# Performance work log

Hardware: AMD Instinct MI355X
Metric: run time of the kernel (lower is better)

Reference implementation:

```python
import jax, jax.numpy as jnp
import numpy as np

B, S, H, P, L, O, E = 32, 1024, 256, 96, 200, 200, 64
N_EULER = 4


def setup_inputs() -> dict:
    key = jax.random.key(0)
    ks = jax.random.split(key, 20)
    def w(k, shape, fan_in):
        return jax.random.normal(k, shape, dtype=jnp.float32) / np.float32(np.sqrt(fan_in))
    return {
        'eco_data': jax.random.normal(ks[0], (B, E), dtype=jnp.float32),
        'tran_data': jax.random.normal(ks[1], (B, S, H), dtype=jnp.float32),
        'tran_data_label': jax.random.normal(ks[2], (B, P, 1), dtype=jnp.float32),
        'time_x': jax.random.uniform(ks[3], (B, S, 1), dtype=jnp.float32),
        'time_y': jax.random.uniform(ks[4], (B, P, 1), dtype=jnp.float32),
        'alpha': jnp.ones((1,), dtype=jnp.float32),
        'W_eco': w(ks[5], (E, H), E), 'b_eco': jnp.zeros((H,), jnp.float32),
        'W_in': w(ks[6], (3, H, L), H), 'W_t': w(ks[7], (3, 1, L), 1), 'b_in': jnp.zeros((3, L), jnp.float32),
        'W_f1': w(ks[8], (3, L, O), L), 'b_f1': jnp.zeros((3, O), jnp.float32),
        'W_f2': w(ks[9], (3, O, L), O), 'b_f2': jnp.zeros((3, L), jnp.float32),
        'W_out': w(ks[10], (3, L, H), L), 'b_out': jnp.zeros((3, H), jnp.float32),
        'W_lin': w(ks[11], (H, P), H), 'b_lin': jnp.zeros((P,), jnp.float32),
    }


def reference(eco_data, tran_data, tran_data_label, time_x, time_y, alpha,
              W_eco, b_eco, W_in, W_t, b_in, W_f1, b_f1, W_f2, b_f2,
              W_out, b_out, W_lin, b_lin):
    S_ = tran_data.shape[1]
    # eco_model: linear encoder [B, E] -> [B, H]
    eco_vec = eco_data @ W_eco + b_eco
    # time features over the observed window (concat then slice, per original)
    time_f = jnp.concatenate([time_x, time_y], axis=1)[:, :S_, :]  # [B, S, 1]
    # ODE_RNN for Q/K/V, stacked on k=3: encode -> Euler ODE solve -> readout
    h = jnp.tanh(jnp.einsum('bsh,khl->kbsl', tran_data, W_in)
                 + jnp.einsum('bst,ktl->kbsl', time_f, W_t)
                 + b_in[:, None, None, :])  # [3, B, S, L]
    dt = jnp.float32(1.0 / N_EULER)
    for _ in range(N_EULER):  # fixed-step Euler solve of tanh-MLP vector field
        hid = jnp.tanh(jnp.einsum('kbsl,klo->kbso', h, W_f1) + b_f1[:, None, None, :])
        f = jnp.einsum('kbso,kol->kbsl', hid, W_f2) + b_f2[:, None, None, :]
        h = h + dt * f
    qkv = (jnp.einsum('kbsl,klh->kbsh', h, W_out) + b_out[:, None, None, :]
           + eco_vec[None, :, None, :])  # [3, B, S, H]
    # zero out padded timesteps (last channel == 0 means padding)
    mask = jnp.where(tran_data[:, :, -1] == 0, 0.0, 1.0)[None, :, :, None]
    qkv = qkv * mask
    Q, K, V = qkv[0], qkv[1], qkv[2]
    scale = jnp.float32(1.0 / np.sqrt(H))
    scores = jnp.einsum('bqh,bkh->bqk', Q, K) * scale  # [B, S, S]
    attn = jax.nn.softmax(scores, axis=-1)
    ctx = jnp.einsum('bqk,bkh->bqh', attn, V)  # [B, S, H]
    out = ctx @ W_lin + b_lin  # [B, S, P]
    return out
```

## Files before the change

kernel.cpp:

```cpp
#include <hip/hip_runtime.h>

constexpr int Bc = 32, Sc = 1024, Hc = 256, Pc = 96, Lc = 200, Oc = 200, Ec = 64;
constexpr int Mtot = Bc * Sc;
constexpr float DT = 0.25f;
constexpr int KP = 224;

enum { MODE_ENC = 0, MODE_QKV = 3, MODE_OUT = 4, MODE_BF16OUT = 5 };

typedef short bf16x8 __attribute__((ext_vector_type(8)));
typedef float f32x4 __attribute__((ext_vector_type(4)));
typedef unsigned short u16x8 __attribute__((ext_vector_type(8)));

__device__ inline unsigned short f2bf(float x) {
    union { float f; unsigned int u; } v; v.f = x;
    unsigned int r = v.u + 0x7FFFu + ((v.u >> 16) & 1u);
    return (unsigned short)(r >> 16);
}
__device__ inline float bf2f(unsigned short x) {
    union { unsigned int u; float f; } v; v.u = ((unsigned int)x) << 16;
    return v.f;
}
__device__ inline float fast_tanh(float x) {
    float cx = fminf(fmaxf(x, -15.f), 15.f);
    float e = __expf(2.f * cx);
    return __fdividef(e - 1.f, e + 1.f);
}

__global__ __launch_bounds__(256) void eco_kernel(
    const float* __restrict__ eco_data, const float* __restrict__ W_eco,
    const float* __restrict__ b_eco, float* __restrict__ eco_vec)
{
    const int b = blockIdx.x, h = threadIdx.x;
    float acc = b_eco[h];
    #pragma unroll
    for (int e = 0; e < Ec; e++)
        acc = fmaf(eco_data[b * Ec + e], W_eco[(size_t)e * Hc + h], acc);
    eco_vec[(size_t)b * Hc + h] = acc;
}

__global__ void wtrans_all(
    const float* __restrict__ W_in, const float* __restrict__ W_f1,
    const float* __restrict__ W_f2, const float* __restrict__ W_out,
    const float* __restrict__ W_lin,
    unsigned short* __restrict__ WinT, unsigned short* __restrict__ Wf1T,
    unsigned short* __restrict__ Wf2T, unsigned short* __restrict__ WoutT,
    unsigned short* __restrict__ WlinT)
{
    const int z = blockIdx.z;
    const int n = blockIdx.x * 16 + threadIdx.x;
    const int k = blockIdx.y * 16 + threadIdx.y;

    const float* W; unsigned short* WT;
    int K, N, Kpad, Npad;
    if (z < 3)       { W = W_in  + (size_t)z * 256 * 200;       WT = WinT  + (size_t)z * 256 * 256;       K = 256; N = 200; Kpad = 256; Npad = 256; }
    else if (z < 6)  { W = W_f1  + (size_t)(z - 3) * 200 * 200; WT = Wf1T  + (size_t)(z - 3) * 224 * 256; K = 200; N = 200; Kpad = 224; Npad = 256; }
    else if (z < 9)  { W = W_f2  + (size_t)(z - 6) * 200 * 200; WT = Wf2T  + (size_t)(z - 6) * 224 * 256; K = 200; N = 200; Kpad = 224; Npad = 256; }
    else if (z < 12) { W = W_out + (size_t)(z - 9) * 200 * 256; WT = WoutT + (size_t)(z - 9) * 224 * 256; K = 200; N = 256; Kpad = 224; Npad = 256; }
    else             { W = W_lin;                               WT = WlinT;                               K = 256; N =  96; Kpad = 256; Npad = 128; }

    if (n >= Npad || k >= Kpad) return;
    float v = (n < N && k < K) ? W[(size_t)k * N + n] : 0.f;
    WT[(size_t)n * Kpad + k] = f2bf(v);
}

template <int MODE, typename TA>
__global__ __launch_bounds__(256) void mfma_gemm(
    const TA* __restrict__ A, const unsigned short* __restrict__ WT,
    const float* __restrict__ bias, void* __restrict__ Cv,
    int M, int N, int K, int Kpad,
    size_t aStrideZ, size_t wStrideZ, size_t bStrideZ, size_t cStrideZ,
    const float* __restrict__ timev, const float* __restrict__ wtv,
    const float* __restrict__ eco, const float* __restrict__ trandat,
    unsigned short* __restrict__ Ck, unsigned short* __restrict__ Cvt)
{
    constexpr int LDS_S = 40;
    __shared__ unsigned short SM[128 * LDS_S * 2];
    unsigned short* As = SM;
    unsigned short* Bs = SM + 128 * LDS_S;

    const int tid = threadIdx.x;
    const int z = blockIdx.z;
    const int m0 = blockIdx.y * 128;
    const int n0 = blockIdx.x * 128;

    A    += (size_t)z * aStrideZ;
    WT   += (size_t)z * wStrideZ;
    bias += (size_t)z * bStrideZ;
    float* Cf = (float*)Cv + (size_t)z * cStrideZ;
    unsigned short* Cu = (unsigned short*)Cv + (size_t)z * cStrideZ;
    const float* wtp = wtv ? (wtv + (size_t)z * Lc) : nullptr;

    const int lane = tid & 63, wave = tid >> 6;
    const int wm = (wave & 1) * 64, wn = (wave >> 1) * 64;
    const int fm = lane & 15, fq = lane >> 4;

    f32x4 acc[4][4];
    #pragma unroll
    for (int i = 0; i < 4; i++)
        #pragma unroll
        for (int j = 0; j < 4; j++)
            acc[i][j] = (f32x4){0.f, 0.f, 0.f, 0.f};

    for (int k0 = 0; k0 < K; k0 += 32) {
        if (k0) __syncthreads();
        #pragma unroll
        for (int i = 0; i < 4; i++) {
            const int f = i * 256 + tid;
            const int row = f >> 3, kq = f & 7;
            const int k = k0 + kq * 4;
            ushort4 s;
            if constexpr (sizeof(TA) == 4) {
                float4 v = {0.f, 0.f, 0.f, 0.f};
                if (k < K) v = *(const float4*)((const float*)A + (size_t)(m0 + row) * K + k);
                s.x = f2bf(v.x); s.y = f2bf(v.y); s.z = f2bf(v.z); s.w = f2bf(v.w);
            } else {
                s = make_ushort4(0, 0, 0, 0);
                if (k < K) s = *(const ushort4*)((const unsigned short*)A + (size_t)(m0 + row) * K + k);
            }
            *(ushort4*)&As[row * LDS_S + kq * 4] = s;
        }
        #pragma unroll
        for (int i = 0; i < 2; i++) {
            const int f = i * 256 + tid;
            const int row = f >> 2, q = f & 3;
            u16x8 v = *(const u16x8*)(WT + (size_t)(n0 + row) * Kpad + k0 + q * 8);
            *(u16x8*)&Bs[row * LDS_S + q * 8] = v;
        }
        __syncthreads();

        bf16x8 af[4], bfr[4];
        #pragma unroll
        for (int mi = 0; mi < 4; mi++)
            af[mi] = *(const bf16x8*)&As[(wm + mi * 16 + fm) * LDS_S + fq * 8];
        #pragma unroll
        for (int nj = 0; nj < 4; nj++)
            bfr[nj] = *(const bf16x8*)&Bs[(wn + nj * 16 + fm) * LDS_S + fq * 8];
        #pragma unroll
        for (int mi = 0; mi < 4; mi++)
            #pragma unroll
            for (int nj = 0; nj < 4; nj++)
                acc[mi][nj] = __builtin_amdgcn_mfma_f32_16x16x32_bf16(
                    af[mi], bfr[nj], acc[mi][nj], 0, 0, 0);
    }

    if (MODE == MODE_QKV && z == 2) {
        constexpr int BSTR = 136;
        const int bq = m0 >> 10, sq0 = m0 & (Sc - 1);
        const int myhalf = wn >> 6;
        #pragma unroll
        for (int half = 0; half < 2; half++) {
            __syncthreads();
            if (myhalf == half) {
                #pragma unroll
                for (int mi = 0; mi < 4; mi++)
                    #pragma unroll
                    for (int nj = 0; nj < 4; nj++) {
                        const int nn = n0 + wn + nj * 16 + fm;
                        const float bv = bias[nn];
                        const float ev = eco[(size_t)bq * Hc + nn];
                        #pragma unroll
                        for (int r = 0; r < 4; r++) {
                            const int mm = m0 + wm + mi * 16 + fq * 4 + r;
                            float v = acc[mi][nj][r] + bv + ev;
                            if (trandat[(size_t)mm * Hc + (Hc - 1)] == 0.f) v = 0.f;
                            SM[(nj * 16 + fm) * BSTR + wm + mi * 16 + fq * 4 + r] = f2bf(v);
                        }
                    }
            }
            __syncthreads();
            #pragma unroll
            for (int i = 0; i < 4; i++) {
                const int vv = i * 256 + tid;
                const int nl = vv >> 4, vc = vv & 15;
                *(u16x8*)&Cvt[((size_t)bq * Hc + n0 + half * 64 + nl) * Sc + sq0 + vc * 8] =
                    *(const u16x8*)&SM[nl * BSTR + vc * 8];
            }
        }
        return;
    }

    #pragma unroll
    for (int mi = 0; mi < 4; mi++) {
        #pragma unroll
        for (int nj = 0; nj < 4; nj++) {
            const int nn = n0 + wn + nj * 16 + fm;
            if (nn >= N) continue;
            const float bv = (MODE == MODE_BF16OUT) ? 0.f
                           : ((MODE == MODE_ENC && nn >= Lc) ? 0.f : bias[nn]);
            #pragma unroll
            for (int r = 0; r < 4; r++) {
                const int mm = m0 + wm + mi * 16 + fq * 4 + r;
                float v = acc[mi][nj][r] + bv;
                if (MODE == MODE_ENC) {
                    float vv = (nn < Lc) ? fast_tanh(v + timev[mm] * wtp[nn]) : 0.f;
                    Cu[(size_t)mm * N + nn] = f2bf(vv);
                } else if (MODE == MODE_QKV) {
                    v += eco[(size_t)(mm >> 10) * Hc + nn];
                    if (trandat[(size_t)mm * Hc + (Hc - 1)] == 0.f) v = 0.f;
                    if (z == 0)      ((unsigned short*)Cv)[(size_t)mm * Hc + nn] = f2bf(v * 0.0625f);
                    else             Ck[(size_t)mm * Hc + nn] = f2bf(v);
                } else if (MODE == MODE_BF16OUT) {
                    Cu[(size_t)mm * N + nn] = f2bf(v);
                } else {
                    Cf[(size_t)mm * N + nn] = v;
                }
            }
        }
    }
}

__global__ __launch_bounds__(512, 2) void euler_fused(
    unsigned short* __restrict__ hg,
    const unsigned short* __restrict__ W1,
    const unsigned short* __restrict__ W2,
    const float* __restrict__ b1g, const float* __restrict__ b2g)
{
    constexpr int HS = 232;
    constexpr int WS = 40;
    extern __shared__ unsigned short lds[];
    unsigned short* hs  = lds;
    unsigned short* wsb[2] = { lds + 29696, lds + 38656 };
    unsigned short* hcb[2] = { lds + 47616, lds + 52736 };

    const int tid = threadIdx.x;
    const int z = blockIdx.y;
    const int m0 = blockIdx.x * 128;
    unsigned short* hrow = hg + ((size_t)z * Mtot + m0) * KP;
    const unsigned short* W1z = W1 + (size_t)z * 256 * KP;
    const unsigned short* W2z = W2 + (size_t)z * 256 * KP;

    const int lane = tid & 63, w = tid >> 6;
    const int wm = (w & 3) * 32, wn = (w >> 2) * 112;
    const int fm = lane & 15, fq = lane >> 4;

    const int sr = tid >> 2, sq = tid & 3;
    const bool s2 = (tid < 384);

    float b1r[7], b2r[7];
    #pragma unroll
    for (int nj = 0; nj < 7; nj++) {
        const int nn = wn + nj * 16 + fm;
        b1r[nj] = (nn < Oc) ? b1g[z * Oc + nn] : 0.f;
        b2r[nj] = (nn < Lc) ? b2g[z * Lc + nn] : 0.f;
    }

    u16x8 pr0, pr1;
    pr0 = *(const u16x8*)&W1z[sr * KP + sq * 8];
    if (s2) pr1 = *(const u16x8*)&W1z[(sr + 128) * KP + sq * 8];

    #pragma unroll
    for (int i = 0; i < 7; i++) {
        const int f = i * 512 + tid;
        const int r = f / 28, c = (f % 28) * 8;
        *(u16x8*)&hs[r * HS + c] = *(const u16x8*)&hrow[(size_t)r * KP + c];
    }

    for (int it = 0; it < 4; it++) {
        __syncthreads();
        *(u16x8*)&wsb[0][sr * WS + sq * 8] = pr0;
        if (s2) *(u16x8*)&wsb[0][(sr + 128) * WS + sq * 8] = pr1;
        pr0 = *(const u16x8*)&W1z[sr * KP + 32 + sq * 8];
        if (s2) pr1 = *(const u16x8*)&W1z[(sr + 128) * KP + 32 + sq * 8];
        __syncthreads();

        f32x4 acc[2][7];
        #pragma unroll
        for (int mi = 0; mi < 2; mi++)
            #pragma unroll
            for (int nj = 0; nj < 7; nj++)
                acc[mi][nj] = (f32x4){0.f, 0.f, 0.f, 0.f};

        for (int k = 0; k < 7; k++) {
            if (k < 6) {
                unsigned short* wb = wsb[(k + 1) & 1];
                *(u16x8*)&wb[sr * WS + sq * 8] = pr0;
                if (s2) *(u16x8*)&wb[(sr + 128) * WS + sq * 8] = pr1;
                const unsigned short* src = (k + 2 < 7) ? (W1z + (k + 2) * 32) : W2z;
                pr0 = *(const u16x8*)&src[sr * KP + sq * 8];
                if (s2) pr1 = *(const u16x8*)&src[(sr + 128) * KP + sq * 8];
            }
            const unsigned short* wr = wsb[k & 1];
            bf16x8 af[2], bfr[7];
            #pragma unroll
            for (int mi = 0; mi < 2; mi++)
                af[mi] = *(const bf16x8*)&hs[(wm + mi * 16 + fm) * HS + k * 32 + fq * 8];
            #pragma unroll
            for (int nj = 0; nj < 7; nj++)
                bfr[nj] = *(const bf16x8*)&wr[(wn + nj * 16 + fm) * WS + fq * 8];
            #pragma unroll
            for (int mi = 0; mi < 2; mi++)
                #pragma unroll
                for (int nj = 0; nj < 7; nj++)
                    acc[mi][nj] = __builtin_amdgcn_mfma_f32_16x16x32_bf16(
                        af[mi], bfr[nj], acc[mi][nj], 0, 0, 0);
            __syncthreads();
        }

        unsigned short hidp[2][7][4];
        #pragma unroll
        for (int mi = 0; mi < 2; mi++)
            #pragma unroll
            for (int nj = 0; nj < 7; nj++)
                #pragma unroll
                for (int r = 0; r < 4; r++)
                    hidp[mi][nj][r] = f2bf(fast_tanh(acc[mi][nj][r] + b1r[nj]));

        {
            *(u16x8*)&wsb[0][sr * WS + sq * 8] = pr0;
            if (s2) *(u16x8*)&wsb[0][(sr + 128) * WS + sq * 8] = pr1;
            pr0 = *(const u16x8*)&W2z[sr * KP + 32 + sq * 8];
            if (s2) pr1 = *(const u16x8*)&W2z[(sr + 128) * KP + 32 + sq * 8];
            #pragma unroll
            for (int t2 = 0; t2 < 2; t2++) {
                const int c0 = t2 * 16;
                if (c0 >= wn && c0 < wn + 112) {
                    const int nj = (c0 - wn) >> 4;
                    #pragma unroll
                    for (int mi = 0; mi < 2; mi++)
                        #pragma unroll
                        for (int r = 0; r < 4; r++)
                            hcb[0][(wm + mi * 16 + fq * 4 + r) * WS + t2 * 16 + fm] =
                                hidp[mi][nj][r];
                }
            }
        }
        __syncthreads();

        f32x4 fac[2][7];
        #pragma unroll
        for (int mi = 0; mi < 2; mi++)
            #pragma unroll
            for (int nj = 0; nj < 7; nj++)
                fac[mi][nj] = (f32x4){0.f, 0.f, 0.f, 0.f};

        for (int k = 0; k < 7; k++) {
            if (k < 6) {
                unsigned short* wb = wsb[(k + 1) & 1];
                unsigned short* hb = hcb[(k + 1) & 1];
                *(u16x8*)&wb[sr * WS + sq * 8] = pr0;
                if (s2) *(u16x8*)&wb[(sr + 128) * WS + sq * 8] = pr1;
                if (k + 2 < 7) {
                    pr0 = *(const u16x8*)&W2z[sr * KP + (k + 2) * 32 + sq * 8];
                    if (s2) pr1 = *(const u16x8*)&W2z[(sr + 128) * KP + (k + 2) * 32 + sq * 8];
                } else if (it != 3) {
                    pr0 = *(const u16x8*)&W1z[sr * KP + sq * 8];
                    if (s2) pr1 = *(const u16x8*)&W1z[(sr + 128) * KP + sq * 8];
                }
                #pragma unroll
                for (int t2 = 0; t2 < 2; t2++) {
                    const int c0 = (k + 1) * 32 + t2 * 16;
                    if (c0 >= wn && c0 < wn + 112) {
                        const int nj = (c0 - wn) >> 4;
                        #pragma unroll
                        for (int mi = 0; mi < 2; mi++)
                            #pragma unroll
                            for (int r = 0; r < 4; r++)
                                hb[(wm + mi * 16 + fq * 4 + r) * WS + t2 * 16 + fm] =
                                    hidp[mi][nj][r];
                    }
                }
            }
            const unsigned short* wr = wsb[k & 1];
            const unsigned short* hr = hcb[k & 1];
            bf16x8 af2[2], bf2[7];
            #pragma unroll
            for (int mi = 0; mi < 2; mi++)
                af2[mi] = *(const bf16x8*)&hr[(wm + mi * 16 + fm) * WS + fq * 8];
            #pragma unroll
            for (int nj = 0; nj < 7; nj++)
                bf2[nj] = *(const bf16x8*)&wr[(wn + nj * 16 + fm) * WS + fq * 8];
            #pragma unroll
            for (int mi = 0; mi < 2; mi++)
                #pragma unroll
                for (int nj = 0; nj < 7; nj++)
                    fac[mi][nj] = __builtin_amdgcn_mfma_f32_16x16x32_bf16(
                        af2[mi], bf2[nj], fac[mi][nj], 0, 0, 0);
            __syncthreads();
        }

        #pragma unroll
        for (int mi = 0; mi < 2; mi++)
            #pragma unroll
            for (int nj = 0; nj < 7; nj++) {
                const int nn = wn + nj * 16 + fm;
                #pragma unroll
                for (int r = 0; r < 4; r++) {
                    const int row = wm + mi * 16 + fq * 4 + r;
                    const float fv = fac[mi][nj][r] + b2r[nj];
                    hs[row * HS + nn] = f2bf(bf2f(hs[row * HS + nn]) + DT * fv);
                }
            }
    }

    __syncthreads();
    #pragma unroll
    for (int i = 0; i < 7; i++) {
        const int f = i * 512 + tid;
        const int r = f / 28, c = (f % 28) * 8;
        *(u16x8*)&hrow[(size_t)r * KP + c] = *(const u16x8*)&hs[r * HS + c];
    }
}

__global__ __launch_bounds__(512) void flash_attn(
    const unsigned short* __restrict__ Qb, const unsigned short* __restrict__ Kb,
    const unsigned short* __restrict__ VT, unsigned short* __restrict__ ctx)
{
    constexpr int QS = 264;
    constexpr int KS = 264;
    constexpr int VS = 72;
    constexpr int PS = 72;
    extern __shared__ unsigned short lds[];
    unsigned short* qs = lds;
    unsigned short* ks = lds + 128 * QS;
    unsigned short* vs = lds + 128 * QS + 64 * KS;
    unsigned short* ps = lds + 128 * QS + 64 * KS + 256 * VS;

    const int tid = threadIdx.x;
    const int b = blockIdx.y, q0 = blockIdx.x * 128;
    const int lane = tid & 63, w = tid >> 6;
    const int fm = lane & 15, fq = lane >> 4;
    unsigned short* psw = ps + w * 16 * PS;

    const unsigned short* Qp = Qb + (size_t)b * Sc * Hc;
    const unsigned short* Kp = Kb + (size_t)b * Sc * Hc;
    const unsigned short* Vp = VT + (size_t)b * Hc * Sc;

    #pragma unroll
    for (int i = 0; i < 8; i++) {
        const int v = i * 512 + tid;
        *(u16x8*)&qs[(v >> 5) * QS + (v & 31) * 8] =
            *(const u16x8*)&Qp[(size_t)(q0 + (v >> 5)) * Hc + (v & 31) * 8];
    }

    f32x4 of[16];
    #pragma unroll
    for (int nj = 0; nj < 16; nj++) of[nj] = (f32x4){0.f, 0.f, 0.f, 0.f};
    float lrun[4] = {0.f, 0.f, 0.f, 0.f};

    for (int c = 0; c < 16; c++) {
        __syncthreads();
        const int s0 = c * 64;
        #pragma unroll
        for (int i = 0; i < 4; i++) {
            const int v = i * 512 + tid;
            *(u16x8*)&ks[(v >> 5) * KS + (v & 31) * 8] =
                *(const u16x8*)&Kp[(size_t)(s0 + (v >> 5)) * Hc + (v & 31) * 8];
            *(u16x8*)&vs[(v >> 3) * VS + (v & 7) * 8] =
                *(const u16x8*)&Vp[(size_t)(v >> 3) * Sc + s0 + (v & 7) * 8];
        }
        __syncthreads();

        f32x4 sc[4];
        #pragma unroll
        for (int nj = 0; nj < 4; nj++) sc[nj] = (f32x4){0.f, 0.f, 0.f, 0.f};
        #pragma unroll
        for (int kc = 0; kc < 8; kc++) {
            const bf16x8 aq = *(const bf16x8*)&qs[(w * 16 + fm) * QS + kc * 32 + fq * 8];
            #pragma unroll
            for (int nj = 0; nj < 4; nj++) {
                const bf16x8 bk = *(const bf16x8*)&ks[(nj * 16 + fm) * KS + kc * 32 + fq * 8];
                sc[nj] = __builtin_amdgcn_mfma_f32_16x16x32_bf16(aq, bk, sc[nj], 0, 0, 0);
            }
        }

        float rsum[4] = {0.f, 0.f, 0.f, 0.f};
        #pragma unroll
        for (int nj = 0; nj < 4; nj++)
            #pragma unroll
            for (int r = 0; r < 4; r++) {
                const float p = __expf(sc[nj][r]);
                rsum[r] += p;
                psw[(fq * 4 + r) * PS + nj * 16 + fm] = f2bf(p);
            }
        #pragma unroll
        for (int r = 0; r < 4; r++) {
            float s = rsum[r];
            #pragma unroll
            for (int o = 8; o > 0; o >>= 1) s += __shfl_xor(s, o, 64);
            lrun[r] += s;
        }

        #pragma unroll
        for (int t = 0; t < 2; t++) {
            const bf16x8 ap = *(const bf16x8*)&psw[fm * PS + t * 32 + fq * 8];
            #pragma unroll
            for (int nj = 0; nj < 16; nj++) {
                const bf16x8 bv = *(const bf16x8*)&vs[(nj * 16 + fm) * VS + t * 32 + fq * 8];
                of[nj] = __builtin_amdgcn_mfma_f32_16x16x32_bf16(ap, bv, of[nj], 0, 0, 0);
            }
        }
    }

    float inv[4];
    #pragma unroll
    for (int r = 0; r < 4; r++) inv[r] = __frcp_rn(lrun[r]);
    #pragma unroll
    for (int nj = 0; nj < 16; nj++)
        #pragma unroll
        for (int r = 0; r < 4; r++)
            ctx[((size_t)b * Sc + q0 + w * 16 + fq * 4 + r) * Hc + nj * 16 + fm] =
                f2bf(of[nj][r] * inv[r]);
}

extern "C" void kernel_launch(void* const* d_in, const int* in_sizes, int n_in,
                              void* d_out, int out_size, void* d_ws, size_t ws_size,
                              hipStream_t stream)
{
    const float* eco_data = (const float*)d_in[0];
    const float* tran     = (const float*)d_in[1];
    const float* time_x   = (const float*)d_in[3];
    const float* W_eco    = (const float*)d_in[6];
    const float* b_eco    = (const float*)d_in[7];
    const float* W_in     = (const float*)d_in[8];
    const float* W_t      = (const float*)d_in[9];
    const float* b_in     = (const float*)d_in[10];
    const float* W_f1     = (const float*)d_in[11];
    const float* b_f1     = (const float*)d_in[12];
    const float* W_f2     = (const float*)d_in[13];
    const float* b_f2     = (const float*)d_in[14];
    const float* W_out    = (const float*)d_in[15];
    const float* b_out    = (const float*)d_in[16];
    const float* W_lin    = (const float*)d_in[17];
    const float* b_lin    = (const float*)d_in[18];
    float* out = (float*)d_out;

    float* eco_vec = (float*)d_ws;
    unsigned short* hpad = (unsigned short*)(eco_vec + 8192);
    unsigned short* Qb = hpad + (size_t)3 * Mtot * KP;
    unsigned short* Kb = Qb + (size_t)Mtot * Hc;
    unsigned short* VT = Kb + (size_t)Mtot * Hc;
    unsigned short* P  = VT + (size_t)Mtot * Hc;
    unsigned short* WinT  = P + (size_t)Mtot * Sc;
    unsigned short* Wf1T  = WinT  + (size_t)3 * 256 * 256;
    unsigned short* Wf2T  = Wf1T  + (size_t)3 * 256 * KP;
    unsigned short* WoutT = Wf2T  + (size_t)3 * 256 * KP;
    unsigned short* WlinT = WoutT + (size_t)3 * 256 * KP;
    unsigned short* ctxb = hpad;

    constexpr int EULER_LDS = 57856 * 2;
    static_assert(EULER_LDS == 115712, "euler lds");
    hipFuncSetAttribute((const void*)euler_fused,
                        hipFuncAttributeMaxDynamicSharedMemorySize, EULER_LDS);
    constexpr int FLASH_LDS = (128 * 264 + 64 * 264 + 256 * 72 + 8 * 16 * 72) * 2;
    static_assert(FLASH_LDS == 156672, "flash lds");
    hipFuncSetAttribute((const void*)flash_attn,
                        hipFuncAttributeMaxDynamicSharedMemorySize, FLASH_LDS);

    eco_kernel<<<Bc, Hc, 0, stream>>>(eco_data, W_eco, b_eco, eco_vec);

    wtrans_all<<<dim3(16, 16, 13), dim3(16, 16), 0, stream>>>(
        W_in, W_f1, W_f2, W_out, W_lin, WinT, Wf1T, Wf2T, WoutT, WlinT);

    const dim3 blk(256);

    mfma_gemm<MODE_ENC, float><<<dim3(2, 256, 3), blk, 0, stream>>>(
        tran, WinT, b_in, hpad, Mtot, KP, Hc, 256,
        0, 65536, Lc, (size_t)Mtot * KP, time_x, W_t, nullptr, nullptr, nullptr, nullptr);

    euler_fused<<<dim3(Mtot / 128, 3), 512, EULER_LDS, stream>>>(
        hpad, Wf1T, Wf2T, b_f1, b_f2);

    mfma_gemm<MODE_QKV, unsigned short><<<dim3(2, 256, 3), blk, 0, stream>>>(
        hpad, WoutT, b_out, Qb, Mtot, Hc, KP, KP,
        (size_t)Mtot * KP, 57344, Hc, 0, nullptr, nullptr, eco_vec, tran, Kb, VT);

    flash_attn<<<dim3(8, 32), 512, FLASH_LDS, stream>>>(Qb, Kb, VT, ctxb);

    mfma_gemm<MODE_OUT, unsigned short><<<dim3(1, 256, 1), blk, 0, stream>>>(
        ctxb, WlinT, b_lin, out, Mtot, Pc, Hc, 256,
        0, 0, 0, 0, nullptr, nullptr, nullptr, nullptr, nullptr, nullptr);
}
```

Measured before the change: 521.5 us.

## Halve Euler kernel row tile to 64 and move biases to LDS for occupancy

The fused Euler kernel now processes 64 rows per block instead of 128, so each wave handles one 16-row MFMA tile instead of two. Accumulator and bias registers drop, and the biases move into shared memory, shrinking LDS from about 113KB to 76KB. Launch bounds are raised to allow more blocks per CU. The cost is that every weight tile streamed through LDS is now reused across half as many rows, which doubles weight traffic and barrier count per row.

```diff
diff --git a/kernel.cpp b/kernel.cpp
--- a/kernel.cpp
+++ b/kernel.cpp
@@ -209,7 +209,7 @@
     }
 }
 
-__global__ __launch_bounds__(512, 2) void euler_fused(
+__global__ __launch_bounds__(512, 4) void euler_fused(
     unsigned short* __restrict__ hg,
     const unsigned short* __restrict__ W1,
     const unsigned short* __restrict__ W2,
@@ -219,29 +219,29 @@
     constexpr int WS = 40;
     extern __shared__ unsigned short lds[];
     unsigned short* hs  = lds;
-    unsigned short* wsb[2] = { lds + 29696, lds + 38656 };
-    unsigned short* hcb[2] = { lds + 47616, lds + 52736 };
+    unsigned short* wsb[2] = { lds + 14848, lds + 23808 };
+    unsigned short* hcb[2] = { lds + 32768, lds + 35328 };
+    float* bs = (float*)(lds + 37888);
 
     const int tid = threadIdx.x;
     const int z = blockIdx.y;
-    const int m0 = blockIdx.x * 128;
+    const int m0 = blockIdx.x * 64;
     unsigned short* hrow = hg + ((size_t)z * Mtot + m0) * KP;
     const unsigned short* W1z = W1 + (size_t)z * 256 * KP;
     const unsigned short* W2z = W2 + (size_t)z * 256 * KP;
 
     const int lane = tid & 63, w = tid >> 6;
-    const int wm = (w & 3) * 32, wn = (w >> 2) * 112;
+    const int wm = (w & 3) * 16, wn = (w >> 2) * 112;
     const int fm = lane & 15, fq = lane >> 4;
 
     const int sr = tid >> 2, sq = tid & 3;
     const bool s2 = (tid < 384);
 
-    float b1r[7], b2r[7];
-    #pragma unroll
-    for (int nj = 0; nj < 7; nj++) {
-        const int nn = wn + nj * 16 + fm;
-        b1r[nj] = (nn < Oc) ? b1g[z * Oc + nn] : 0.f;
-        b2r[nj] = (nn < Lc) ? b2g[z * Lc + nn] : 0.f;
+    if (tid < 448) {
+        float v;
+        if (tid < 224) v = (tid < Oc) ? b1g[z * Oc + tid] : 0.f;
+        else { const int t = tid - 224; v = (t < Lc) ? b2g[z * Lc + t] : 0.f; }
+        bs[tid] = v;
     }
 
     u16x8 pr0, pr1;
@@ -249,10 +249,12 @@
     if (s2) pr1 = *(const u16x8*)&W1z[(sr + 128) * KP + sq * 8];
 
     #pragma unroll
-    for (int i = 0; i < 7; i++) {
+    for (int i = 0; i < 4; i++) {
         const int f = i * 512 + tid;
-        const int r = f / 28, c = (f % 28) * 8;
-        *(u16x8*)&hs[r * HS + c] = *(const u16x8*)&hrow[(size_t)r * KP + c];
+        if (f < 1792) {
+            const int r = f / 28, c = (f % 28) * 8;
+            *(u16x8*)&hs[r * HS + c] = *(const u16x8*)&hrow[(size_t)r * KP + c];
+        }
     }
 
     for (int it = 0; it < 4; it++) {
@@ -263,12 +265,10 @@
         if (s2) pr1 = *(const u16x8*)&W1z[(sr + 128) * KP + 32 + sq * 8];
         __syncthreads();
 
-        f32x4 acc[2][7];
-        #pragma unroll
-        for (int mi = 0; mi < 2; mi++)
-            #pragma unroll
-            for (int nj = 0; nj < 7; nj++)
-                acc[mi][nj] = (f32x4){0.f, 0.f, 0.f, 0.f};
+        f32x4 acc[7];
+        #pragma unroll
+        for (int nj = 0; nj < 7; nj++)
+            acc[nj] = (f32x4){0.f, 0.f, 0.f, 0.f};
 
         for (int k = 0; k < 7; k++) {
             if (k < 6) {
@@ -280,30 +280,26 @@
                 if (s2) pr1 = *(const u16x8*)&src[(sr + 128) * KP + sq * 8];
             }
             const unsigned short* wr = wsb[k & 1];
-            bf16x8 af[2], bfr[7];
-            #pragma unroll
-            for (int mi = 0; mi < 2; mi++)
-                af[mi] = *(const bf16x8*)&hs[(wm + mi * 16 + fm) * HS + k * 32 + fq * 8];
+            const bf16x8 af = *(const bf16x8*)&hs[(wm + fm) * HS + k * 32 + fq * 8];
+            bf16x8 bfr[7];
             #pragma unroll
             for (int nj = 0; nj < 7; nj++)
                 bfr[nj] = *(const bf16x8*)&wr[(wn + nj * 16 + fm) * WS + fq * 8];
             #pragma unroll
-            for (int mi = 0; mi < 2; mi++)
-                #pragma unroll
-                for (int nj = 0; nj < 7; nj++)
-                    acc[mi][nj] = __builtin_amdgcn_mfma_f32_16x16x32_bf16(
-                        af[mi], bfr[nj], acc[mi][nj], 0, 0, 0);
+            for (int nj = 0; nj < 7; nj++)
+                acc[nj] = __builtin_amdgcn_mfma_f32_16x16x32_bf16(
+                    af, bfr[nj], acc[nj], 0, 0, 0);
             __syncthreads();
         }
 
-        unsigned short hidp[2][7][4];
-        #pragma unroll
-        for (int mi = 0; mi < 2; mi++)
-            #pragma unroll
-            for (int nj = 0; nj < 7; nj++)
-                #pragma unroll
-                for (int r = 0; r < 4; r++)
-                    hidp[mi][nj][r] = f2bf(fast_tanh(acc[mi][nj][r] + b1r[nj]));
+        unsigned short hidp[7][4];
+        #pragma unroll
+        for (int nj = 0; nj < 7; nj++) {
+            const float b1v = bs[wn + nj * 16 + fm];
+            #pragma unroll
+            for (int r = 0; r < 4; r++)
+                hidp[nj][r] = f2bf(fast_tanh(acc[nj][r] + b1v));
+        }
 
         {
             *(u16x8*)&wsb[0][sr * WS + sq * 8] = pr0;
@@ -316,22 +312,17 @@
                 if (c0 >= wn && c0 < wn + 112) {
                     const int nj = (c0 - wn) >> 4;
                     #pragma unroll
-                    for (int mi = 0; mi < 2; mi++)
-                        #pragma unroll
-                        for (int r = 0; r < 4; r++)
-                            hcb[0][(wm + mi * 16 + fq * 4 + r) * WS + t2 * 16 + fm] =
-                                hidp[mi][nj][r];
+                    for (int r = 0; r < 4; r++)
+                        hcb[0][(wm + fq * 4 + r) * WS + t2 * 16 + fm] = hidp[nj][r];
                 }
             }
         }
         __syncthreads();
 
-        f32x4 fac[2][7];
-        #pragma unroll
-        for (int mi = 0; mi < 2; mi++)
-            #pragma unroll
-            for (int nj = 0; nj < 7; nj++)
-                fac[mi][nj] = (f32x4){0.f, 0.f, 0.f, 0.f};
+        f32x4 fac[7];
+        #pragma unroll
+        for (int nj = 0; nj < 7; nj++)
+            fac[nj] = (f32x4){0.f, 0.f, 0.f, 0.f};
 
         for (int k = 0; k < 7; k++) {
             if (k < 6) {
@@ -352,52 +343,46 @@
                     if (c0 >= wn && c0 < wn + 112) {
                         const int nj = (c0 - wn) >> 4;
                         #pragma unroll
-                        for (int mi = 0; mi < 2; mi++)
-                            #pragma unroll
-                            for (int r = 0; r < 4; r++)
-                                hb[(wm + mi * 16 + fq * 4 + r) * WS + t2 * 16 + fm] =
-                                    hidp[mi][nj][r];
+                        for (int r = 0; r < 4; r++)
+                            hb[(wm + fq * 4 + r) * WS + t2 * 16 + fm] = hidp[nj][r];
                     }
                 }
             }
             const unsigned short* wr = wsb[k & 1];
             const unsigned short* hr = hcb[k & 1];
-            bf16x8 af2[2], bf2[7];
-            #pragma unroll
-            for (int mi = 0; mi < 2; mi++)
-                af2[mi] = *(const bf16x8*)&hr[(wm + mi * 16 + fm) * WS + fq * 8];
+            const bf16x8 af2 = *(const bf16x8*)&hr[(wm + fm) * WS + fq * 8];
+            bf16x8 bf2[7];
             #pragma unroll
             for (int nj = 0; nj < 7; nj++)
                 bf2[nj] = *(const bf16x8*)&wr[(wn + nj * 16 + fm) * WS + fq * 8];
             #pragma unroll
-            for (int mi = 0; mi < 2; mi++)
-                #pragma unroll
-                for (int nj = 0; nj < 7; nj++)
-                    fac[mi][nj] = __builtin_amdgcn_mfma_f32_16x16x32_bf16(
-                        af2[mi], bf2[nj], fac[mi][nj], 0, 0, 0);
+            for (int nj = 0; nj < 7; nj++)
+                fac[nj] = __builtin_amdgcn_mfma_f32_16x16x32_bf16(
+                    af2, bf2[nj], fac[nj], 0, 0, 0);
             __syncthreads();
         }
 
         #pragma unroll
-        for (int mi = 0; mi < 2; mi++)
-            #pragma unroll
-            for (int nj = 0; nj < 7; nj++) {
-                const int nn = wn + nj * 16 + fm;
-                #pragma unroll
-                for (int r = 0; r < 4; r++) {
-                    const int row = wm + mi * 16 + fq * 4 + r;
-                    const float fv = fac[mi][nj][r] + b2r[nj];
-                    hs[row * HS + nn] = f2bf(bf2f(hs[row * HS + nn]) + DT * fv);
-                }
-            }
+        for (int nj = 0; nj < 7; nj++) {
+            const int nn = wn + nj * 16 + fm;
+            const float b2v = bs[224 + nn];
+            #pragma unroll
+            for (int r = 0; r < 4; r++) {
+                const int row = wm + fq * 4 + r;
+                const float fv = fac[nj][r] + b2v;
+                hs[row * HS + nn] = f2bf(bf2f(hs[row * HS + nn]) + DT * fv);
+            }
+        }
     }
 
     __syncthreads();
     #pragma unroll
-    for (int i = 0; i < 7; i++) {
+    for (int i = 0; i < 4; i++) {
         const int f = i * 512 + tid;
-        const int r = f / 28, c = (f % 28) * 8;
-        *(u16x8*)&hrow[(size_t)r * KP + c] = *(const u16x8*)&hs[r * HS + c];
+        if (f < 1792) {
+            const int r = f / 28, c = (f % 28) * 8;
+            *(u16x8*)&hrow[(size_t)r * KP + c] = *(const u16x8*)&hs[r * HS + c];
+        }
     }
 }
 
@@ -537,8 +522,8 @@
     unsigned short* WlinT = WoutT + (size_t)3 * 256 * KP;
     unsigned short* ctxb = hpad;
 
-    constexpr int EULER_LDS = 57856 * 2;
-    static_assert(EULER_LDS == 115712, "euler lds");
+    constexpr int EULER_LDS = (14848 + 2 * 8960 + 2 * 2560) * 2 + 448 * 4;
+    static_assert(EULER_LDS == 77568, "euler lds");
     hipFuncSetAttribute((const void*)euler_fused,
                         hipFuncAttributeMaxDynamicSharedMemorySize, EULER_LDS);
     constexpr int FLASH_LDS = (128 * 264 + 64 * 264 + 256 * 72 + 8 * 16 * 72) * 2;
@@ -557,7 +542,7 @@
         tran, WinT, b_in, hpad, Mtot, KP, Hc, 256,
         0, 65536, Lc, (size_t)Mtot * KP, time_x, W_t, nullptr, nullptr, nullptr, nullptr);
 
-    euler_fused<<<dim3(Mtot / 128, 3), 512, EULER_LDS, stream>>>(
+    euler_fused<<<dim3(Mtot / 64, 3), 512, EULER_LDS, stream>>>(
         hpad, Wf1T, Wf2T, b_f1, b_f2);
 
     mfma_gemm<MODE_QKV, unsigned short><<<dim3(2, 256, 3), blk, 0, stream>>>(
```

Measured after the change: 568.2 us. 1.09x slower.

## Double-buffer K/V tiles in flash attention with register-resident Q

Applied to the files above, without the earlier changes.

Restructures the flash attention kernel so Q fragments stay in registers rather than LDS. K and V are streamed in 32-key chunks through a double-buffered LDS ring, with global loads for the next chunk issued before the current chunk's MFMAs. This cuts LDS footprint and leaves one barrier per iteration instead of two, aiming to hide global load latency. The trade-off is twice as many loop iterations with smaller MFMA batches and more register pressure from the prefetch and Q registers.

```diff
diff --git a/kernel.cpp b/kernel.cpp
--- a/kernel.cpp
+++ b/kernel.cpp
@@ -405,15 +405,13 @@
     const unsigned short* __restrict__ Qb, const unsigned short* __restrict__ Kb,
     const unsigned short* __restrict__ VT, unsigned short* __restrict__ ctx)
 {
-    constexpr int QS = 264;
-    constexpr int KS = 264;
-    constexpr int VS = 72;
-    constexpr int PS = 72;
+    constexpr int KS = 260;
+    constexpr int VS = 68;
+    constexpr int PS = 36;
     extern __shared__ unsigned short lds[];
-    unsigned short* qs = lds;
-    unsigned short* ks = lds + 128 * QS;
-    unsigned short* vs = lds + 128 * QS + 64 * KS;
-    unsigned short* ps = lds + 128 * QS + 64 * KS + 256 * VS;
+    unsigned short* ks = lds;
+    unsigned short* vs = lds + 2 * 32 * KS;
+    unsigned short* ps = lds + 2 * 32 * KS + 2 * 256 * VS;
 
     const int tid = threadIdx.x;
     const int b = blockIdx.y, q0 = blockIdx.x * 128;
@@ -425,53 +423,69 @@
     const unsigned short* Kp = Kb + (size_t)b * Sc * Hc;
     const unsigned short* Vp = VT + (size_t)b * Hc * Sc;
 
-    #pragma unroll
-    for (int i = 0; i < 8; i++) {
-        const int v = i * 512 + tid;
-        *(u16x8*)&qs[(v >> 5) * QS + (v & 31) * 8] =
-            *(const u16x8*)&Qp[(size_t)(q0 + (v >> 5)) * Hc + (v & 31) * 8];
-    }
+    bf16x8 aq[8];
+    #pragma unroll
+    for (int kc = 0; kc < 8; kc++)
+        aq[kc] = *(const bf16x8*)&Qp[(size_t)(q0 + w * 16 + fm) * Hc + kc * 32 + fq * 8];
+
+    const int kr = tid >> 5, kcol = (tid & 31) * 8;
+    const int vr = tid >> 2, vcol = (tid & 3) * 8;
+    const unsigned short* KgA = Kp + (size_t)kr * Hc + kcol;
+    const unsigned short* KgB = KgA + (size_t)16 * Hc;
+    const unsigned short* VgA = Vp + (size_t)vr * Sc + vcol;
+    const unsigned short* VgB = VgA + (size_t)128 * Sc;
+    const int kwA = kr * KS + kcol, kwB = (kr + 16) * KS + kcol;
+    const int vwA = vr * VS + vcol, vwB = (vr + 128) * VS + vcol;
+
+    {
+        u16x8 a0 = *(const u16x8*)KgA;
+        u16x8 a1 = *(const u16x8*)KgB;
+        u16x8 b0 = *(const u16x8*)VgA;
+        u16x8 b1 = *(const u16x8*)VgB;
+        *(u16x8*)&ks[kwA] = a0; *(u16x8*)&ks[kwB] = a1;
+        *(u16x8*)&vs[vwA] = b0; *(u16x8*)&vs[vwB] = b1;
+    }
+    __syncthreads();
 
     f32x4 of[16];
     #pragma unroll
     for (int nj = 0; nj < 16; nj++) of[nj] = (f32x4){0.f, 0.f, 0.f, 0.f};
     float lrun[4] = {0.f, 0.f, 0.f, 0.f};
 
-    for (int c = 0; c < 16; c++) {
-        __syncthreads();
-        const int s0 = c * 64;
-        #pragma unroll
-        for (int i = 0; i < 4; i++) {
-            const int v = i * 512 + tid;
-            *(u16x8*)&ks[(v >> 5) * KS + (v & 31) * 8] =
-                *(const u16x8*)&Kp[(size_t)(s0 + (v >> 5)) * Hc + (v & 31) * 8];
-            *(u16x8*)&vs[(v >> 3) * VS + (v & 7) * 8] =
-                *(const u16x8*)&Vp[(size_t)(v >> 3) * Sc + s0 + (v & 7) * 8];
-        }
-        __syncthreads();
-
-        f32x4 sc[4];
-        #pragma unroll
-        for (int nj = 0; nj < 4; nj++) sc[nj] = (f32x4){0.f, 0.f, 0.f, 0.f};
+    int cur = 0;
+    for (int c = 0; c < 32; c++) {
+        u16x8 nk0, nk1, nv0, nv1;
+        if (c < 31) {
+            const size_t ko = (size_t)(c + 1) * 32 * Hc;
+            const size_t vo = (size_t)(c + 1) * 32;
+            nk0 = *(const u16x8*)(KgA + ko);
+            nk1 = *(const u16x8*)(KgB + ko);
+            nv0 = *(const u16x8*)(VgA + vo);
+            nv1 = *(const u16x8*)(VgB + vo);
+        }
+
+        const unsigned short* ksc = ks + cur * (32 * KS);
+        const unsigned short* vsc = vs + cur * (256 * VS);
+
+        f32x4 s0v = (f32x4){0.f, 0.f, 0.f, 0.f};
+        f32x4 s1v = (f32x4){0.f, 0.f, 0.f, 0.f};
         #pragma unroll
         for (int kc = 0; kc < 8; kc++) {
-            const bf16x8 aq = *(const bf16x8*)&qs[(w * 16 + fm) * QS + kc * 32 + fq * 8];
-            #pragma unroll
-            for (int nj = 0; nj < 4; nj++) {
-                const bf16x8 bk = *(const bf16x8*)&ks[(nj * 16 + fm) * KS + kc * 32 + fq * 8];
-                sc[nj] = __builtin_amdgcn_mfma_f32_16x16x32_bf16(aq, bk, sc[nj], 0, 0, 0);
-            }
-        }
-
-        float rsum[4] = {0.f, 0.f, 0.f, 0.f};
-        #pragma unroll
-        for (int nj = 0; nj < 4; nj++)
-            #pragma unroll
-            for (int r = 0; r < 4; r++) {
-                const float p = __expf(sc[nj][r]);
-                rsum[r] += p;
-                psw[(fq * 4 + r) * PS + nj * 16 + fm] = f2bf(p);
-            }
+            const bf16x8 bk0 = *(const bf16x8*)&ksc[fm * KS + kc * 32 + fq * 8];
+            const bf16x8 bk1 = *(const bf16x8*)&ksc[(16 + fm) * KS + kc * 32 + fq * 8];
+            s0v = __builtin_amdgcn_mfma_f32_16x16x32_bf16(aq[kc], bk0, s0v, 0, 0, 0);
+            s1v = __builtin_amdgcn_mfma_f32_16x16x32_bf16(aq[kc], bk1, s1v, 0, 0, 0);
+        }
+
+        float rsum[4];
+        #pragma unroll
+        for (int r = 0; r < 4; r++) {
+            const float p0 = __expf(s0v[r]);
+            const float p1 = __expf(s1v[r]);
+            rsum[r] = p0 + p1;
+            psw[(fq * 4 + r) * PS + fm] = f2bf(p0);
+            psw[(fq * 4 + r) * PS + 16 + fm] = f2bf(p1);
+        }
         #pragma unroll
         for (int r = 0; r < 4; r++) {
             float s = rsum[r];
@@ -480,15 +494,21 @@
             lrun[r] += s;
         }
 
-        #pragma unroll
-        for (int t = 0; t < 2; t++) {
-            const bf16x8 ap = *(const bf16x8*)&psw[fm * PS + t * 32 + fq * 8];
-            #pragma unroll
-            for (int nj = 0; nj < 16; nj++) {
-                const bf16x8 bv = *(const bf16x8*)&vs[(nj * 16 + fm) * VS + t * 32 + fq * 8];
-                of[nj] = __builtin_amdgcn_mfma_f32_16x16x32_bf16(ap, bv, of[nj], 0, 0, 0);
-            }
-        }
+        const bf16x8 ap = *(const bf16x8*)&psw[fm * PS + fq * 8];
+        #pragma unroll
+        for (int nj = 0; nj < 16; nj++) {
+            const bf16x8 bv = *(const bf16x8*)&vsc[(nj * 16 + fm) * VS + fq * 8];
+            of[nj] = __builtin_amdgcn_mfma_f32_16x16x32_bf16(ap, bv, of[nj], 0, 0, 0);
+        }
+
+        if (c < 31) {
+            unsigned short* ksn = ks + (cur ^ 1) * (32 * KS);
+            unsigned short* vsn = vs + (cur ^ 1) * (256 * VS);
+            *(u16x8*)&ksn[kwA] = nk0; *(u16x8*)&ksn[kwB] = nk1;
+            *(u16x8*)&vsn[vwA] = nv0; *(u16x8*)&vsn[vwB] = nv1;
+        }
+        __syncthreads();
+        cur ^= 1;
     }
 
     float inv[4];
@@ -541,8 +561,8 @@
     static_assert(EULER_LDS == 115712, "euler lds");
     hipFuncSetAttribute((const void*)euler_fused,
                         hipFuncAttributeMaxDynamicSharedMemorySize, EULER_LDS);
-    constexpr int FLASH_LDS = (128 * 264 + 64 * 264 + 256 * 72 + 8 * 16 * 72) * 2;
-    static_assert(FLASH_LDS == 156672, "flash lds");
+    constexpr int FLASH_LDS = (2 * 32 * 260 + 2 * 256 * 68 + 8 * 16 * 36) * 2;
+    static_assert(FLASH_LDS == 112128, "flash lds");
     hipFuncSetAttribute((const void*)flash_attn,
                         hipFuncAttributeMaxDynamicSharedMemorySize, FLASH_LDS);
 
```

After: 714.7 us. +37.1%, slower.
